# Optimization experiments

Measured on AMD Instinct MI355X. Metric: run time of the kernel, lower is better.

## Reference

```python
import jax, jax.numpy as jnp
import numpy as np

N_NODES = 100000


def gcn_conv(x, edge_index, W, b, n_nodes):
    """PyG GCNConv: add self-loops, symmetric deg norm, linear, scatter-add, bias."""
    self_loops = jnp.arange(n_nodes, dtype=edge_index.dtype)
    src = jnp.concatenate([edge_index[0], self_loops])  # [E+N]
    dst = jnp.concatenate([edge_index[1], self_loops])  # [E+N]
    xw = x @ W  # [N, out]
    deg = jax.ops.segment_sum(jnp.ones_like(dst, dtype=xw.dtype), dst, num_segments=n_nodes)
    deg_inv_sqrt = jnp.where(deg > 0, jax.lax.rsqrt(deg), 0.0)
    norm = deg_inv_sqrt[src] * deg_inv_sqrt[dst]  # [E+N]
    msg = xw[src] * norm[:, None]                 # [E+N, out]
    out = jax.ops.segment_sum(msg, dst, num_segments=n_nodes)
    return out + b


def setup_inputs() -> dict:
    key = jax.random.key(0)
    ks = jax.random.split(key, 8)
    n, e, d_in, h = N_NODES, 3200000, 128, 16
    x = jax.random.normal(ks[0], (n, d_in), dtype=jnp.float32)
    edge_index = jax.random.randint(ks[1], (2, e), 0, n, dtype=jnp.int64)
    W1 = jax.random.normal(ks[2], (d_in, h), dtype=jnp.float32) / np.sqrt(d_in)
    b1 = jnp.zeros((h,), dtype=jnp.float32)
    W2 = jax.random.normal(ks[3], (h, h), dtype=jnp.float32) / np.sqrt(h)
    b2 = jnp.zeros((h,), dtype=jnp.float32)
    W_lin = jax.random.normal(ks[4], (h, 1), dtype=jnp.float32) / np.sqrt(h)
    b_lin = jnp.zeros((1,), dtype=jnp.float32)
    return {"x": x, "edge_index": edge_index, "W1": W1, "b1": b1,
            "W2": W2, "b2": b2, "W_lin": W_lin, "b_lin": b_lin}


def reference(x, edge_index, W1, b1, W2, b2, W_lin, b_lin):
    n = x.shape[0]
    h = gcn_conv(x, edge_index, W1, b1, n)
    h = jax.nn.relu(h)
    # dropout is identity in eval mode (training=False)
    h = gcn_conv(h, edge_index, W2, b2, n)
    h = jax.nn.relu(h)
    out = h @ W_lin + b_lin  # [N, 1]
    return out.squeeze(-1)   # [N]
```

## Files before the change

kernel.cpp:

```cpp
#include <hip/hip_runtime.h>

#define DIN 128
#define HDIM 16
#define NB 256
#define BDIV_MAX 416
#define CAP 13312
#define BIN_EPT 16

__device__ __forceinline__ float4 f4add(float4 a, float4 b) {
    return make_float4(a.x + b.x, a.y + b.y, a.z + b.z, a.w + b.w);
}

__device__ __forceinline__ int load_idx(const void* ei, long long i, int is64) {
    return is64 ? (int)((const long long*)ei)[i] : ((const int*)ei)[i];
}

__global__ __launch_bounds__(256) void k_main(const void* __restrict__ ei, long long E,
                                              int bdiv, int* __restrict__ bcur,
                                              unsigned int* __restrict__ recs,
                                              const float* __restrict__ x,
                                              const float* __restrict__ W1,
                                              float* __restrict__ y1,
                                              int n, int nbin) {
    __shared__ int cnt[NB];
    __shared__ int base[NB];
    __shared__ float Ws[DIN * HDIM];
    int tid = threadIdx.x;
    if ((int)blockIdx.x < nbin) {
        unsigned probe = ((const unsigned*)ei)[1 + 2 * (tid & 63)];
        int is64 = (__ballot(probe != 0) == 0ull) ? 1 : 0;
        if (tid < NB) cnt[tid] = 0;
        __syncthreads();
        long long e0 = (long long)blockIdx.x * (256 * BIN_EPT);
        int s[BIN_EPT], d[BIN_EPT], b[BIN_EPT];
#pragma unroll
        for (int i = 0; i < BIN_EPT; i++) {
            long long e = e0 + (long long)i * 256 + tid;
            if (e < E) {
                s[i] = load_idx(ei, e, is64);
                d[i] = load_idx(ei, E + e, is64);
                b[i] = (int)((unsigned)d[i] / (unsigned)bdiv);
                atomicAdd(&cnt[b[i]], 1);
            } else {
                b[i] = -1;
            }
        }
        __syncthreads();
        if (tid < NB) {
            base[tid] = atomicAdd(&bcur[tid], cnt[tid]);
            cnt[tid] = 0;
        }
        __syncthreads();
#pragma unroll
        for (int i = 0; i < BIN_EPT; i++) {
            if (b[i] >= 0) {
                int off = atomicAdd(&cnt[b[i]], 1);
                int pos = base[b[i]] + off;
                if (pos < CAP) {
                    unsigned int dloc = (unsigned)(d[i] - b[i] * bdiv);
                    recs[(size_t)b[i] * CAP + pos] = (dloc << 18) | (unsigned)s[i];
                }
            }
        }
    } else {
        for (int i = tid; i < DIN * HDIM; i += 256) Ws[i] = W1[i];
        __syncthreads();
        int node = ((int)blockIdx.x - nbin) * 256 + tid;
        if (node >= n) return;
        float acc[HDIM];
#pragma unroll
        for (int f = 0; f < HDIM; f++) acc[f] = 0.f;
        const float4* xr = (const float4*)(x + (size_t)node * DIN);
#pragma unroll 8
        for (int k4 = 0; k4 < DIN / 4; k4++) {
            float4 xv = xr[k4];
            int k = k4 * 4;
#pragma unroll
            for (int f = 0; f < HDIM; f++) {
                acc[f] += xv.x * Ws[(k + 0) * HDIM + f];
                acc[f] += xv.y * Ws[(k + 1) * HDIM + f];
                acc[f] += xv.z * Ws[(k + 2) * HDIM + f];
                acc[f] += xv.w * Ws[(k + 3) * HDIM + f];
            }
        }
        float4* yr = (float4*)(y1 + (size_t)node * HDIM);
#pragma unroll
        for (int q = 0; q < 4; q++)
            yr[q] = make_float4(acc[q * 4 + 0], acc[q * 4 + 1],
                                acc[q * 4 + 2], acc[q * 4 + 3]);
    }
}

__global__ __launch_bounds__(512) void k_prep(const unsigned int* __restrict__ recs,
                                              const int* __restrict__ bcur,
                                              float* __restrict__ dis,
                                              unsigned int* __restrict__ meta,
                                              int* __restrict__ col,
                                              float* __restrict__ y1,
                                              int bdiv, int n) {
    __shared__ int cnt_sh[BDIV_MAX];
    __shared__ int sc[512];
    __shared__ unsigned short buf[CAP];
    int tid = threadIdx.x;
    int b = blockIdx.x;
    int lo = b * bdiv; if (lo > n) lo = n;
    int hi = lo + bdiv; if (hi > n) hi = n;
    int nd = hi - lo;
    if (tid < nd) cnt_sh[tid] = 0;
    __syncthreads();
    int m = bcur[b]; if (m > CAP) m = CAP;
    const unsigned int* r = recs + (size_t)b * CAP;
    for (int i = tid; i < m; i += 512)
        atomicAdd(&cnt_sh[r[i] >> 18], 1);
    __syncthreads();
    int v = (tid < nd) ? cnt_sh[tid] : 0;
    sc[tid] = v;
    __syncthreads();
    for (int off = 1; off < 512; off <<= 1) {
        int t = (tid >= off) ? sc[tid - off] : 0;
        __syncthreads();
        sc[tid] += t;
        __syncthreads();
    }
    float dv_t = 0.f;
    if (tid < nd) {
        int excl = sc[tid] - v;
        dv_t = rsqrtf((float)v + 1.0f);
        dis[lo + tid] = dv_t;
        meta[lo + tid] = ((unsigned)(b * CAP + excl) << 10) | (unsigned)v;
        cnt_sh[tid] = excl;
    }
    __syncthreads();
    for (int i = tid; i < m; i += 512) {
        int pos = atomicAdd(&cnt_sh[r[i] >> 18], 1);
        buf[pos] = (unsigned short)i;
    }
    __syncthreads();
    for (int i = tid; i < m; i += 512)
        col[b * CAP + i] = (int)(r[buf[i]] & 0x3FFFFu);
    int q = tid & 3;
    int slot = tid >> 2;
    float4* yv = (float4*)y1;
    for (int j = slot; j < nd; j += 128) {
        float dvj = __shfl(dv_t, 0, 1);
        (void)dvj;
        int node = lo + j;
        float dv = dis[node];
        float4 t = yv[(size_t)node * 4 + q];
        yv[(size_t)node * 4 + q] =
            make_float4(t.x * dv, t.y * dv, t.z * dv, t.w * dv);
    }
}

__global__ __launch_bounds__(256) void k_gather1(const unsigned int* __restrict__ meta,
                                                 const int* __restrict__ col,
                                                 const float* __restrict__ y1,
                                                 const float* __restrict__ dis,
                                                 const float* __restrict__ b1,
                                                 const float* __restrict__ W2,
                                                 float* __restrict__ y2, int n) {
    __shared__ float4 Ws4[HDIM][4];
    if (threadIdx.x < HDIM * 4)
        ((float4*)Ws4)[threadIdx.x] = ((const float4*)W2)[threadIdx.x];
    __syncthreads();
    int ln = threadIdx.x >> 2;
    int q  = threadIdx.x & 3;
    int node = blockIdx.x * 64 + ln;
    if (node >= n) return;
    unsigned mt = meta[node];
    int start = (int)(mt >> 10);
    int end   = start + (int)(mt & 1023u);
    const float4* yv = (const float4*)y1;
    float4 a0 = make_float4(0.f, 0.f, 0.f, 0.f), a1 = a0, a2 = a0, a3 = a0;
    int e = start;
    for (; e + 16 <= end; e += 16) {
        int c0 = col[e + q], c1 = col[e + 4 + q],
            c2 = col[e + 8 + q], c3 = col[e + 12 + q];
        int s[16];
#pragma unroll
        for (int k = 0; k < 4; k++) {
            s[k]      = __shfl(c0, k, 4);
            s[4 + k]  = __shfl(c1, k, 4);
            s[8 + k]  = __shfl(c2, k, 4);
            s[12 + k] = __shfl(c3, k, 4);
        }
        float4 v[16];
#pragma unroll
        for (int k = 0; k < 16; k++) v[k] = yv[(size_t)s[k] * 4 + q];
#pragma unroll
        for (int k = 0; k < 16; k += 4) {
            a0 = f4add(a0, v[k + 0]); a1 = f4add(a1, v[k + 1]);
            a2 = f4add(a2, v[k + 2]); a3 = f4add(a3, v[k + 3]);
        }
    }
    for (; e + 4 <= end; e += 4) {
        int c0 = col[e + q];
        int s0 = __shfl(c0, 0, 4), s1 = __shfl(c0, 1, 4),
            s2 = __shfl(c0, 2, 4), s3 = __shfl(c0, 3, 4);
        float4 v0 = yv[(size_t)s0 * 4 + q];
        float4 v1 = yv[(size_t)s1 * 4 + q];
        float4 v2 = yv[(size_t)s2 * 4 + q];
        float4 v3 = yv[(size_t)s3 * 4 + q];
        a0 = f4add(a0, v0); a1 = f4add(a1, v1);
        a2 = f4add(a2, v2); a3 = f4add(a3, v3);
    }
    for (; e < end; e++)
        a0 = f4add(a0, yv[(size_t)col[e] * 4 + q]);
    float4 acc = f4add(f4add(a0, a1), f4add(a2, a3));
    acc = f4add(acc, yv[(size_t)node * 4 + q]);
    float dv = dis[node];
    float4 bb = ((const float4*)b1)[q];
    float4 h;
    h.x = fmaxf(dv * acc.x + bb.x, 0.f);
    h.y = fmaxf(dv * acc.y + bb.y, 0.f);
    h.z = fmaxf(dv * acc.z + bb.z, 0.f);
    h.w = fmaxf(dv * acc.w + bb.w, 0.f);
    float4 o = make_float4(0.f, 0.f, 0.f, 0.f);
#pragma unroll
    for (int k = 0; k < 4; k++) {
        float4 hk;
        hk.x = __shfl(h.x, k, 4); hk.y = __shfl(h.y, k, 4);
        hk.z = __shfl(h.z, k, 4); hk.w = __shfl(h.w, k, 4);
        float hv[4] = {hk.x, hk.y, hk.z, hk.w};
#pragma unroll
        for (int c = 0; c < 4; c++) {
            float4 w = Ws4[k * 4 + c][q];
            o.x += hv[c] * w.x; o.y += hv[c] * w.y;
            o.z += hv[c] * w.z; o.w += hv[c] * w.w;
        }
    }
    ((float4*)y2)[(size_t)node * 4 + q] =
        make_float4(o.x * dv, o.y * dv, o.z * dv, o.w * dv);
}

__global__ __launch_bounds__(256) void k_gather2(const unsigned int* __restrict__ meta,
                                                 const int* __restrict__ col,
                                                 const float* __restrict__ y2,
                                                 const float* __restrict__ dis,
                                                 const float* __restrict__ b2,
                                                 const float* __restrict__ Wlin,
                                                 const float* __restrict__ blin,
                                                 float* __restrict__ out, int n) {
    int ln = threadIdx.x >> 2;
    int q  = threadIdx.x & 3;
    int node = blockIdx.x * 64 + ln;
    if (node >= n) return;
    unsigned mt = meta[node];
    int start = (int)(mt >> 10);
    int end   = start + (int)(mt & 1023u);
    const float4* yv = (const float4*)y2;
    float4 a0 = make_float4(0.f, 0.f, 0.f, 0.f), a1 = a0, a2 = a0, a3 = a0;
    int e = start;
    for (; e + 16 <= end; e += 16) {
        int c0 = col[e + q], c1 = col[e + 4 + q],
            c2 = col[e + 8 + q], c3 = col[e + 12 + q];
        int s[16];
#pragma unroll
        for (int k = 0; k < 4; k++) {
            s[k]      = __shfl(c0, k, 4);
            s[4 + k]  = __shfl(c1, k, 4);
            s[8 + k]  = __shfl(c2, k, 4);
            s[12 + k] = __shfl(c3, k, 4);
        }
        float4 v[16];
#pragma unroll
        for (int k = 0; k < 16; k++) v[k] = yv[(size_t)s[k] * 4 + q];
#pragma unroll
        for (int k = 0; k < 16; k += 4) {
            a0 = f4add(a0, v[k + 0]); a1 = f4add(a1, v[k + 1]);
            a2 = f4add(a2, v[k + 2]); a3 = f4add(a3, v[k + 3]);
        }
    }
    for (; e + 4 <= end; e += 4) {
        int c0 = col[e + q];
        int s0 = __shfl(c0, 0, 4), s1 = __shfl(c0, 1, 4),
            s2 = __shfl(c0, 2, 4), s3 = __shfl(c0, 3, 4);
        float4 v0 = yv[(size_t)s0 * 4 + q];
        float4 v1 = yv[(size_t)s1 * 4 + q];
        float4 v2 = yv[(size_t)s2 * 4 + q];
        float4 v3 = yv[(size_t)s3 * 4 + q];
        a0 = f4add(a0, v0); a1 = f4add(a1, v1);
        a2 = f4add(a2, v2); a3 = f4add(a3, v3);
    }
    for (; e < end; e++)
        a0 = f4add(a0, yv[(size_t)col[e] * 4 + q]);
    float4 acc = f4add(f4add(a0, a1), f4add(a2, a3));
    acc = f4add(acc, yv[(size_t)node * 4 + q]);
    float dv = dis[node];
    float4 bb = ((const float4*)b2)[q];
    float4 wl = ((const float4*)Wlin)[q];
    float v = 0.f;
    v += fmaxf(dv * acc.x + bb.x, 0.f) * wl.x;
    v += fmaxf(dv * acc.y + bb.y, 0.f) * wl.y;
    v += fmaxf(dv * acc.z + bb.z, 0.f) * wl.z;
    v += fmaxf(dv * acc.w + bb.w, 0.f) * wl.w;
    v += __shfl_xor(v, 1, 4);
    v += __shfl_xor(v, 2, 4);
    if (q == 0) out[node] = v + blin[0];
}

extern "C" void kernel_launch(void* const* d_in, const int* in_sizes, int n_in,
                              void* d_out, int out_size, void* d_ws, size_t ws_size,
                              hipStream_t stream) {
    const float* x    = (const float*)d_in[0];
    const void*  ei   = d_in[1];
    const float* W1   = (const float*)d_in[2];
    const float* b1   = (const float*)d_in[3];
    const float* W2   = (const float*)d_in[4];
    const float* b2   = (const float*)d_in[5];
    const float* Wlin = (const float*)d_in[6];
    const float* blin = (const float*)d_in[7];
    float* out = (float*)d_out;

    const int n = in_sizes[0] / DIN;
    const long long E = in_sizes[1] / 2;
    const int bdiv = (n + NB - 1) / NB;

    char* ws = (char*)d_ws;
    size_t off = 0;
    auto alloc = [&](size_t bytes) { char* p = ws + off; off += (bytes + 255) & ~(size_t)255; return p; };
    int*   bcur   = (int*)alloc(NB * 4);
    float* dis    = (float*)alloc((size_t)n * 4);
    unsigned int* meta = (unsigned int*)alloc((size_t)n * 4);
    float* y1     = (float*)alloc((size_t)n * HDIM * 4);
    size_t region_elems = (size_t)NB * CAP;
    if (region_elems < (size_t)n * HDIM) region_elems = (size_t)n * HDIM;
    char*  region = alloc(region_elems * 4);
    unsigned int* recs = (unsigned int*)region;
    float* y2     = (float*)region;
    int*   col    = (int*)alloc((size_t)NB * CAP * 4);

    const int nb_xw  = (n + 255) / 256;
    const int nb_bin = (int)((E + 256 * BIN_EPT - 1) / (256 * BIN_EPT));
    const int nb_g   = (n + 63) / 64;

    hipMemsetAsync(bcur, 0, NB * sizeof(int), stream);
    k_main<<<nb_bin + nb_xw, 256, 0, stream>>>(ei, E, bdiv, bcur, recs, x, W1, y1, n, nb_bin);
    k_prep<<<NB, 512, 0, stream>>>(recs, bcur, dis, meta, col, y1, bdiv, n);
    k_gather1<<<nb_g, 256, 0, stream>>>(meta, col, y1, dis, b1, W2, y2, n);
    k_gather2<<<nb_g, 256, 0, stream>>>(meta, col, y2, dis, b2, Wlin, blin, out, n);
}
```

Baseline: 229.8 us.

## Fuse all GCN stages into one persistent cooperative kernel with grid syncs

Replaces the memset plus four separate kernel launches with a single cooperative persistent kernel that runs binning/XW, bucket prep, and both gathers as phases separated by grid-wide syncs. Bucket count grows from 256 to 512 with a smaller per-bucket capacity, blocks go to 512 threads, and the gather unroll drops from 16 to 8. The aim is to remove launch gaps and tail effects between stages. The cost is grid-sync overhead and a grid capped at 1024 blocks, which may limit parallelism in the gather phases. The old multi-kernel path is kept as a fallback if the cooperative launch fails.

```diff
diff --git a/kernel.cpp b/kernel.cpp
--- a/kernel.cpp
+++ b/kernel.cpp
@@ -1,11 +1,13 @@
 #include <hip/hip_runtime.h>
+#include <hip/hip_cooperative_groups.h>
+
+namespace cg = cooperative_groups;
 
 #define DIN 128
 #define HDIM 16
-#define NB 256
-#define BDIV_MAX 416
-#define CAP 13312
-#define BIN_EPT 16
+#define NB2 512
+#define CAP2 7168
+#define SMEM_BYTES 18432
 
 __device__ __forceinline__ float4 f4add(float4 a, float4 b) {
     return make_float4(a.x + b.x, a.y + b.y, a.z + b.z, a.w + b.w);
@@ -15,101 +17,86 @@
     return is64 ? (int)((const long long*)ei)[i] : ((const int*)ei)[i];
 }
 
-__global__ __launch_bounds__(256) void k_main(const void* __restrict__ ei, long long E,
-                                              int bdiv, int* __restrict__ bcur,
-                                              unsigned int* __restrict__ recs,
-                                              const float* __restrict__ x,
-                                              const float* __restrict__ W1,
-                                              float* __restrict__ y1,
-                                              int n, int nbin) {
-    __shared__ int cnt[NB];
-    __shared__ int base[NB];
-    __shared__ float Ws[DIN * HDIM];
-    int tid = threadIdx.x;
-    if ((int)blockIdx.x < nbin) {
-        unsigned probe = ((const unsigned*)ei)[1 + 2 * (tid & 63)];
-        int is64 = (__ballot(probe != 0) == 0ull) ? 1 : 0;
-        if (tid < NB) cnt[tid] = 0;
-        __syncthreads();
-        long long e0 = (long long)blockIdx.x * (256 * BIN_EPT);
-        int s[BIN_EPT], d[BIN_EPT], b[BIN_EPT];
-#pragma unroll
-        for (int i = 0; i < BIN_EPT; i++) {
-            long long e = e0 + (long long)i * 256 + tid;
-            if (e < E) {
-                s[i] = load_idx(ei, e, is64);
-                d[i] = load_idx(ei, E + e, is64);
-                b[i] = (int)((unsigned)d[i] / (unsigned)bdiv);
-                atomicAdd(&cnt[b[i]], 1);
-            } else {
-                b[i] = -1;
+__device__ __forceinline__ void bin_unit(int u, int tid, char* smem,
+        const void* ei, long long E, int bdiv, int* bcur, unsigned* recs) {
+    int* cnt  = (int*)smem;
+    int* base = cnt + 512;
+    unsigned probe = ((const unsigned*)ei)[1 + 2 * (tid & 63)];
+    int is64 = (__ballot(probe != 0) == 0ull) ? 1 : 0;
+    cnt[tid] = 0;
+    __syncthreads();
+    long long e0 = (long long)u * 4096;
+    int s[8], d[8], bb[8];
+#pragma unroll
+    for (int i = 0; i < 8; i++) {
+        long long e = e0 + i * 512 + tid;
+        if (e < E) {
+            s[i] = load_idx(ei, e, is64);
+            d[i] = load_idx(ei, E + e, is64);
+            bb[i] = (int)((unsigned)d[i] / (unsigned)bdiv);
+            atomicAdd(&cnt[bb[i]], 1);
+        } else bb[i] = -1;
+    }
+    __syncthreads();
+    base[tid] = atomicAdd(&bcur[tid], cnt[tid]);
+    cnt[tid] = 0;
+    __syncthreads();
+#pragma unroll
+    for (int i = 0; i < 8; i++) {
+        if (bb[i] >= 0) {
+            int off = atomicAdd(&cnt[bb[i]], 1);
+            int pos = base[bb[i]] + off;
+            if (pos < CAP2) {
+                unsigned dloc = (unsigned)(d[i] - bb[i] * bdiv);
+                recs[(size_t)bb[i] * CAP2 + pos] = (dloc << 18) | (unsigned)s[i];
             }
         }
-        __syncthreads();
-        if (tid < NB) {
-            base[tid] = atomicAdd(&bcur[tid], cnt[tid]);
-            cnt[tid] = 0;
-        }
-        __syncthreads();
-#pragma unroll
-        for (int i = 0; i < BIN_EPT; i++) {
-            if (b[i] >= 0) {
-                int off = atomicAdd(&cnt[b[i]], 1);
-                int pos = base[b[i]] + off;
-                if (pos < CAP) {
-                    unsigned int dloc = (unsigned)(d[i] - b[i] * bdiv);
-                    recs[(size_t)b[i] * CAP + pos] = (dloc << 18) | (unsigned)s[i];
-                }
-            }
-        }
-    } else {
-        for (int i = tid; i < DIN * HDIM; i += 256) Ws[i] = W1[i];
-        __syncthreads();
-        int node = ((int)blockIdx.x - nbin) * 256 + tid;
-        if (node >= n) return;
-        float acc[HDIM];
-#pragma unroll
-        for (int f = 0; f < HDIM; f++) acc[f] = 0.f;
-        const float4* xr = (const float4*)(x + (size_t)node * DIN);
+    }
+}
+
+__device__ __forceinline__ void xw_unit(int urel, int tid, char* smem,
+        const float* x, const float* W1, float* y1, int n) {
+    float* Ws = (float*)smem;
+    for (int i = tid; i < DIN * HDIM; i += 512) Ws[i] = W1[i];
+    __syncthreads();
+    int node = urel * 512 + tid;
+    if (node >= n) return;
+    float acc[HDIM];
+#pragma unroll
+    for (int f = 0; f < HDIM; f++) acc[f] = 0.f;
+    const float4* xr = (const float4*)(x + (size_t)node * DIN);
 #pragma unroll 8
-        for (int k4 = 0; k4 < DIN / 4; k4++) {
-            float4 xv = xr[k4];
-            int k = k4 * 4;
-#pragma unroll
-            for (int f = 0; f < HDIM; f++) {
-                acc[f] += xv.x * Ws[(k + 0) * HDIM + f];
-                acc[f] += xv.y * Ws[(k + 1) * HDIM + f];
-                acc[f] += xv.z * Ws[(k + 2) * HDIM + f];
-                acc[f] += xv.w * Ws[(k + 3) * HDIM + f];
-            }
-        }
-        float4* yr = (float4*)(y1 + (size_t)node * HDIM);
-#pragma unroll
-        for (int q = 0; q < 4; q++)
-            yr[q] = make_float4(acc[q * 4 + 0], acc[q * 4 + 1],
-                                acc[q * 4 + 2], acc[q * 4 + 3]);
-    }
-}
-
-__global__ __launch_bounds__(512) void k_prep(const unsigned int* __restrict__ recs,
-                                              const int* __restrict__ bcur,
-                                              float* __restrict__ dis,
-                                              unsigned int* __restrict__ meta,
-                                              int* __restrict__ col,
-                                              float* __restrict__ y1,
-                                              int bdiv, int n) {
-    __shared__ int cnt_sh[BDIV_MAX];
-    __shared__ int sc[512];
-    __shared__ unsigned short buf[CAP];
-    int tid = threadIdx.x;
-    int b = blockIdx.x;
+    for (int k4 = 0; k4 < DIN / 4; k4++) {
+        float4 xv = xr[k4];
+        int k = k4 * 4;
+#pragma unroll
+        for (int f = 0; f < HDIM; f++) {
+            acc[f] += xv.x * Ws[(k + 0) * HDIM + f];
+            acc[f] += xv.y * Ws[(k + 1) * HDIM + f];
+            acc[f] += xv.z * Ws[(k + 2) * HDIM + f];
+            acc[f] += xv.w * Ws[(k + 3) * HDIM + f];
+        }
+    }
+    float4* yr = (float4*)(y1 + (size_t)node * HDIM);
+#pragma unroll
+    for (int q = 0; q < 4; q++)
+        yr[q] = make_float4(acc[q * 4 + 0], acc[q * 4 + 1],
+                            acc[q * 4 + 2], acc[q * 4 + 3]);
+}
+
+__device__ __forceinline__ void prep_bucket(int b, int tid, char* smem,
+        const unsigned* recs, const int* bcur, float* dis, unsigned* meta,
+        int* col, float* y1, int bdiv, int n) {
+    int* cnt_sh = (int*)smem;
+    int* sc     = cnt_sh + 512;
+    unsigned short* buf = (unsigned short*)(sc + 512);
     int lo = b * bdiv; if (lo > n) lo = n;
     int hi = lo + bdiv; if (hi > n) hi = n;
     int nd = hi - lo;
     if (tid < nd) cnt_sh[tid] = 0;
     __syncthreads();
-    int m = bcur[b]; if (m > CAP) m = CAP;
-    const unsigned int* r = recs + (size_t)b * CAP;
+    int m = bcur[b]; if (m > CAP2) m = CAP2;
+    const unsigned* r = recs + (size_t)b * CAP2;
     for (int i = tid; i < m; i += 512)
         atomicAdd(&cnt_sh[r[i] >> 18], 1);
     __syncthreads();
@@ -122,12 +109,10 @@
         sc[tid] += t;
         __syncthreads();
     }
-    float dv_t = 0.f;
     if (tid < nd) {
         int excl = sc[tid] - v;
-        dv_t = rsqrtf((float)v + 1.0f);
-        dis[lo + tid] = dv_t;
-        meta[lo + tid] = ((unsigned)(b * CAP + excl) << 10) | (unsigned)v;
+        dis[lo + tid] = rsqrtf((float)v + 1.0f);
+        meta[lo + tid] = ((unsigned)(b * CAP2 + excl) << 10) | (unsigned)v;
         cnt_sh[tid] = excl;
     }
     __syncthreads();
@@ -137,13 +122,10 @@
     }
     __syncthreads();
     for (int i = tid; i < m; i += 512)
-        col[b * CAP + i] = (int)(r[buf[i]] & 0x3FFFFu);
-    int q = tid & 3;
-    int slot = tid >> 2;
+        col[b * CAP2 + i] = (int)(r[buf[i]] & 0x3FFFFu);
+    int q = tid & 3, slot = tid >> 2;
     float4* yv = (float4*)y1;
     for (int j = slot; j < nd; j += 128) {
-        float dvj = __shfl(dv_t, 0, 1);
-        (void)dvj;
         int node = lo + j;
         float dv = dis[node];
         float4 t = yv[(size_t)node * 4 + q];
@@ -152,20 +134,11 @@
     }
 }
 
-__global__ __launch_bounds__(256) void k_gather1(const unsigned int* __restrict__ meta,
-                                                 const int* __restrict__ col,
-                                                 const float* __restrict__ y1,
-                                                 const float* __restrict__ dis,
-                                                 const float* __restrict__ b1,
-                                                 const float* __restrict__ W2,
-                                                 float* __restrict__ y2, int n) {
-    __shared__ float4 Ws4[HDIM][4];
-    if (threadIdx.x < HDIM * 4)
-        ((float4*)Ws4)[threadIdx.x] = ((const float4*)W2)[threadIdx.x];
-    __syncthreads();
-    int ln = threadIdx.x >> 2;
-    int q  = threadIdx.x & 3;
-    int node = blockIdx.x * 64 + ln;
+__device__ __forceinline__ void gather1_unit(int u, int tid, const float4* ws4,
+        const unsigned* meta, const int* col, const float* y1,
+        const float* dis, const float* b1, float* y2, int n) {
+    int ln = tid >> 2, q = tid & 3;
+    int node = u * 128 + ln;
     if (node >= n) return;
     unsigned mt = meta[node];
     int start = (int)(mt >> 10);
@@ -173,25 +146,21 @@
     const float4* yv = (const float4*)y1;
     float4 a0 = make_float4(0.f, 0.f, 0.f, 0.f), a1 = a0, a2 = a0, a3 = a0;
     int e = start;
-    for (; e + 16 <= end; e += 16) {
-        int c0 = col[e + q], c1 = col[e + 4 + q],
-            c2 = col[e + 8 + q], c3 = col[e + 12 + q];
-        int s[16];
+    for (; e + 8 <= end; e += 8) {
+        int c0 = col[e + q], c1 = col[e + 4 + q];
+        int s[8];
 #pragma unroll
         for (int k = 0; k < 4; k++) {
-            s[k]      = __shfl(c0, k, 4);
-            s[4 + k]  = __shfl(c1, k, 4);
-            s[8 + k]  = __shfl(c2, k, 4);
-            s[12 + k] = __shfl(c3, k, 4);
-        }
-        float4 v[16];
-#pragma unroll
-        for (int k = 0; k < 16; k++) v[k] = yv[(size_t)s[k] * 4 + q];
-#pragma unroll
-        for (int k = 0; k < 16; k += 4) {
-            a0 = f4add(a0, v[k + 0]); a1 = f4add(a1, v[k + 1]);
-            a2 = f4add(a2, v[k + 2]); a3 = f4add(a3, v[k + 3]);
-        }
+            s[k]     = __shfl(c0, k, 4);
+            s[4 + k] = __shfl(c1, k, 4);
+        }
+        float4 v[8];
+#pragma unroll
+        for (int k = 0; k < 8; k++) v[k] = yv[(size_t)s[k] * 4 + q];
+        a0 = f4add(a0, v[0]); a1 = f4add(a1, v[1]);
+        a2 = f4add(a2, v[2]); a3 = f4add(a3, v[3]);
+        a0 = f4add(a0, v[4]); a1 = f4add(a1, v[5]);
+        a2 = f4add(a2, v[6]); a3 = f4add(a3, v[7]);
     }
     for (; e + 4 <= end; e += 4) {
         int c0 = col[e + q];
@@ -224,7 +193,7 @@
         float hv[4] = {hk.x, hk.y, hk.z, hk.w};
 #pragma unroll
         for (int c = 0; c < 4; c++) {
-            float4 w = Ws4[k * 4 + c][q];
+            float4 w = ws4[(k * 4 + c) * 4 + q];
             o.x += hv[c] * w.x; o.y += hv[c] * w.y;
             o.z += hv[c] * w.z; o.w += hv[c] * w.w;
         }
@@ -233,17 +202,12 @@
         make_float4(o.x * dv, o.y * dv, o.z * dv, o.w * dv);
 }
 
-__global__ __launch_bounds__(256) void k_gather2(const unsigned int* __restrict__ meta,
-                                                 const int* __restrict__ col,
-                                                 const float* __restrict__ y2,
-                                                 const float* __restrict__ dis,
-                                                 const float* __restrict__ b2,
-                                                 const float* __restrict__ Wlin,
-                                                 const float* __restrict__ blin,
-                                                 float* __restrict__ out, int n) {
-    int ln = threadIdx.x >> 2;
-    int q  = threadIdx.x & 3;
-    int node = blockIdx.x * 64 + ln;
+__device__ __forceinline__ void gather2_unit(int u, int tid,
+        const unsigned* meta, const int* col, const float* y2,
+        const float* dis, const float* b2, const float* Wlin,
+        const float* blin, float* out, int n) {
+    int ln = tid >> 2, q = tid & 3;
+    int node = u * 128 + ln;
     if (node >= n) return;
     unsigned mt = meta[node];
     int start = (int)(mt >> 10);
@@ -251,25 +215,21 @@
     const float4* yv = (const float4*)y2;
     float4 a0 = make_float4(0.f, 0.f, 0.f, 0.f), a1 = a0, a2 = a0, a3 = a0;
     int e = start;
-    for (; e + 16 <= end; e += 16) {
-        int c0 = col[e + q], c1 = col[e + 4 + q],
-            c2 = col[e + 8 + q], c3 = col[e + 12 + q];
-        int s[16];
+    for (; e + 8 <= end; e += 8) {
+        int c0 = col[e + q], c1 = col[e + 4 + q];
+        int s[8];
 #pragma unroll
         for (int k = 0; k < 4; k++) {
-            s[k]      = __shfl(c0, k, 4);
-            s[4 + k]  = __shfl(c1, k, 4);
-            s[8 + k]  = __shfl(c2, k, 4);
-            s[12 + k] = __shfl(c3, k, 4);
-        }
-        float4 v[16];
-#pragma unroll
-        for (int k = 0; k < 16; k++) v[k] = yv[(size_t)s[k] * 4 + q];
-#pragma unroll
-        for (int k = 0; k < 16; k += 4) {
-            a0 = f4add(a0, v[k + 0]); a1 = f4add(a1, v[k + 1]);
-            a2 = f4add(a2, v[k + 2]); a3 = f4add(a3, v[k + 3]);
-        }
+            s[k]     = __shfl(c0, k, 4);
+            s[4 + k] = __shfl(c1, k, 4);
+        }
+        float4 v[8];
+#pragma unroll
+        for (int k = 0; k < 8; k++) v[k] = yv[(size_t)s[k] * 4 + q];
+        a0 = f4add(a0, v[0]); a1 = f4add(a1, v[1]);
+        a2 = f4add(a2, v[2]); a3 = f4add(a3, v[3]);
+        a0 = f4add(a0, v[4]); a1 = f4add(a1, v[5]);
+        a2 = f4add(a2, v[6]); a3 = f4add(a3, v[7]);
     }
     for (; e + 4 <= end; e += 4) {
         int c0 = col[e + q];
@@ -299,44 +259,135 @@
     if (q == 0) out[node] = v + blin[0];
 }
 
+__global__ __launch_bounds__(512, 4) void k_mega(
+        const void* ei, long long E, int bdiv, int* bcur,
+        unsigned* recs ,
+        const float* x, const float* W1, float* y1,
+        float* dis, unsigned* meta, int* col,
+        const float* b1, const float* W2,
+        const float* b2, const float* Wlin, const float* blin,
+        float* out, int n, int nbin, int nxw) {
+    __shared__ __align__(16) char smem[SMEM_BYTES];
+    cg::grid_group g = cg::this_grid();
+    int tid = threadIdx.x, bid = blockIdx.x, gsz = gridDim.x;
+    for (int i = bid * 512 + tid; i < NB2; i += gsz * 512) bcur[i] = 0;
+    g.sync();
+    int total = nbin + nxw;
+    for (int u = bid; u < total; u += gsz) {
+        if (u < nbin) bin_unit(u, tid, smem, ei, E, bdiv, bcur, recs);
+        else          xw_unit(u - nbin, tid, smem, x, W1, y1, n);
+        __syncthreads();
+    }
+    g.sync();
+    for (int b = bid; b < NB2; b += gsz) {
+        prep_bucket(b, tid, smem, recs, bcur, dis, meta, col, y1, bdiv, n);
+        __syncthreads();
+    }
+    g.sync();
+    float4* ws4 = (float4*)smem;
+    if (tid < 64) ws4[tid] = ((const float4*)W2)[tid];
+    __syncthreads();
+    float* y2 = (float*)recs;
+    int units = (n + 127) >> 7;
+    for (int u = bid; u < units; u += gsz)
+        gather1_unit(u, tid, ws4, meta, col, y1, dis, b1, y2, n);
+    g.sync();
+    for (int u = bid; u < units; u += gsz)
+        gather2_unit(u, tid, meta, col, y2, dis, b2, Wlin, blin, out, n);
+}
+
+__global__ __launch_bounds__(512) void f_main(const void* ei, long long E,
+        int bdiv, int* bcur, unsigned* recs, const float* x,
+        const float* W1, float* y1, int n, int nbin) {
+    __shared__ __align__(16) char smem[SMEM_BYTES];
+    int u = blockIdx.x;
+    if (u < nbin) bin_unit(u, threadIdx.x, smem, ei, E, bdiv, bcur, recs);
+    else          xw_unit(u - nbin, threadIdx.x, smem, x, W1, y1, n);
+}
+
+__global__ __launch_bounds__(512) void f_prep(const unsigned* recs,
+        const int* bcur, float* dis, unsigned* meta, int* col,
+        float* y1, int bdiv, int n) {
+    __shared__ __align__(16) char smem[SMEM_BYTES];
+    prep_bucket(blockIdx.x, threadIdx.x, smem, recs, bcur, dis, meta, col,
+                y1, bdiv, n);
+}
+
+__global__ __launch_bounds__(512) void f_g1(const unsigned* meta,
+        const int* col, const float* y1, const float* dis,
+        const float* b1, const float* W2, float* y2, int n) {
+    __shared__ __align__(16) float4 ws4[64];
+    if (threadIdx.x < 64) ws4[threadIdx.x] = ((const float4*)W2)[threadIdx.x];
+    __syncthreads();
+    gather1_unit(blockIdx.x, threadIdx.x, ws4, meta, col, y1, dis, b1, y2, n);
+}
+
+__global__ __launch_bounds__(512) void f_g2(const unsigned* meta,
+        const int* col, const float* y2, const float* dis,
+        const float* b2, const float* Wlin, const float* blin,
+        float* out, int n) {
+    gather2_unit(blockIdx.x, threadIdx.x, meta, col, y2, dis, b2, Wlin,
+                 blin, out, n);
+}
+
 extern "C" void kernel_launch(void* const* d_in, const int* in_sizes, int n_in,
                               void* d_out, int out_size, void* d_ws, size_t ws_size,
                               hipStream_t stream) {
     const float* x    = (const float*)d_in[0];
     const void*  ei   = d_in[1];
+    const float* b1   = (const float*)d_in[3];
     const float* W1   = (const float*)d_in[2];
-    const float* b1   = (const float*)d_in[3];
     const float* W2   = (const float*)d_in[4];
     const float* b2   = (const float*)d_in[5];
     const float* Wlin = (const float*)d_in[6];
     const float* blin = (const float*)d_in[7];
     float* out = (float*)d_out;
 
-    const int n = in_sizes[0] / DIN;
-    const long long E = in_sizes[1] / 2;
-    const int bdiv = (n + NB - 1) / NB;
+    int n = in_sizes[0] / DIN;
+    long long E = in_sizes[1] / 2;
+    int bdiv = (n + NB2 - 1) / NB2;
 
     char* ws = (char*)d_ws;
     size_t off = 0;
     auto alloc = [&](size_t bytes) { char* p = ws + off; off += (bytes + 255) & ~(size_t)255; return p; };
-    int*   bcur   = (int*)alloc(NB * 4);
-    float* dis    = (float*)alloc((size_t)n * 4);
-    unsigned int* meta = (unsigned int*)alloc((size_t)n * 4);
-    float* y1     = (float*)alloc((size_t)n * HDIM * 4);
-    size_t region_elems = (size_t)NB * CAP;
+    int*      bcur = (int*)alloc(NB2 * 4);
+    float*    dis  = (float*)alloc((size_t)n * 4);
+    unsigned* meta = (unsigned*)alloc((size_t)n * 4);
+    float*    y1   = (float*)alloc((size_t)n * HDIM * 4);
+    size_t region_elems = (size_t)NB2 * CAP2;
     if (region_elems < (size_t)n * HDIM) region_elems = (size_t)n * HDIM;
-    char*  region = alloc(region_elems * 4);
-    unsigned int* recs = (unsigned int*)region;
-    float* y2     = (float*)region;
-    int*   col    = (int*)alloc((size_t)NB * CAP * 4);
-
-    const int nb_xw  = (n + 255) / 256;
-    const int nb_bin = (int)((E + 256 * BIN_EPT - 1) / (256 * BIN_EPT));
-    const int nb_g   = (n + 63) / 64;
-
-    hipMemsetAsync(bcur, 0, NB * sizeof(int), stream);
-    k_main<<<nb_bin + nb_xw, 256, 0, stream>>>(ei, E, bdiv, bcur, recs, x, W1, y1, n, nb_bin);
-    k_prep<<<NB, 512, 0, stream>>>(recs, bcur, dis, meta, col, y1, bdiv, n);
-    k_gather1<<<nb_g, 256, 0, stream>>>(meta, col, y1, dis, b1, W2, y2, n);
-    k_gather2<<<nb_g, 256, 0, stream>>>(meta, col, y2, dis, b2, Wlin, blin, out, n);
-}
+    char* region = alloc(region_elems * 4);
+    unsigned* recs = (unsigned*)region;
+    int*      col  = (int*)alloc((size_t)NB2 * CAP2 * 4);
+
+    int nbin  = (int)((E + 4095) / 4096);
+    int nxw   = (n + 511) / 512;
+    int units = (n + 127) / 128;
+
+    void* args[] = { (void*)&ei, (void*)&E, (void*)&bdiv, (void*)&bcur,
+                     (void*)&recs, (void*)&x, (void*)&W1, (void*)&y1,
+                     (void*)&dis, (void*)&meta, (void*)&col,
+                     (void*)&b1, (void*)&W2, (void*)&b2, (void*)&Wlin,
+                     (void*)&blin, (void*)&out, (void*)&n, (void*)&nbin,
+                     (void*)&nxw };
+
+    int nbpc = 0;
+    hipError_t occ = hipOccupancyMaxActiveBlocksPerMultiprocessor(
+        &nbpc, (const void*)k_mega, 512, 0);
+    int grid = (occ == hipSuccess && nbpc > 0) ? nbpc * 256 : 256;
+    if (grid > 1024) grid = 1024;
+
+    hipError_t st = hipLaunchCooperativeKernel((void*)k_mega, dim3(grid),
+                                               dim3(512), args, 0, stream);
+    if (st != hipSuccess) {
+        hipMemsetAsync(bcur, 0, NB2 * sizeof(int), stream);
+        f_main<<<nbin + nxw, 512, 0, stream>>>(ei, E, bdiv, bcur, recs,
+                                               x, W1, y1, n, nbin);
+        f_prep<<<NB2, 512, 0, stream>>>(recs, bcur, dis, meta, col, y1,
+                                        bdiv, n);
+        f_g1<<<units, 512, 0, stream>>>(meta, col, y1, dis, b1, W2,
+                                        (float*)recs, n);
+        f_g2<<<units, 512, 0, stream>>>(meta, col, (float*)recs, dis, b2,
+                                        Wlin, blin, out, n);
+    }
+}
```

Result: slower. 386.2 us (+68.1%).

## Pad CSR rows to multiples of four with a zero dummy node

Applied to the files above, without the earlier changes.

Each node's adjacency row in the CSR built in k_prep is padded to a multiple of four entries. Padding slots point to an extra all-zero row at index n, which is added to y1 and y2. The gather kernels can then load column indices as aligned int4 vectors and drop the scalar tail loop. The cost is extra sentinel-fill work in prep, a slightly larger col buffer, and wasted gathers of the zero row.

```diff
diff --git a/kernel.cpp b/kernel.cpp
--- a/kernel.cpp
+++ b/kernel.cpp
@@ -3,8 +3,8 @@
 #define DIN 128
 #define HDIM 16
 #define NB 256
-#define BDIV_MAX 416
 #define CAP 13312
+#define CAPC 14848
 #define BIN_EPT 16
 
 __device__ __forceinline__ float4 f4add(float4 a, float4 b) {
@@ -66,7 +66,14 @@
         for (int i = tid; i < DIN * HDIM; i += 256) Ws[i] = W1[i];
         __syncthreads();
         int node = ((int)blockIdx.x - nbin) * 256 + tid;
-        if (node >= n) return;
+        if (node > n) return;
+        float4* yr = (float4*)(y1 + (size_t)node * HDIM);
+        if (node == n) {
+            float4 z = make_float4(0.f, 0.f, 0.f, 0.f);
+#pragma unroll
+            for (int q = 0; q < 4; q++) yr[q] = z;
+            return;
+        }
         float acc[HDIM];
 #pragma unroll
         for (int f = 0; f < HDIM; f++) acc[f] = 0.f;
@@ -83,7 +90,6 @@
                 acc[f] += xv.w * Ws[(k + 3) * HDIM + f];
             }
         }
-        float4* yr = (float4*)(y1 + (size_t)node * HDIM);
 #pragma unroll
         for (int q = 0; q < 4; q++)
             yr[q] = make_float4(acc[q * 4 + 0], acc[q * 4 + 1],
@@ -98,23 +104,24 @@
                                               int* __restrict__ col,
                                               float* __restrict__ y1,
                                               int bdiv, int n) {
-    __shared__ int cnt_sh[BDIV_MAX];
+    __shared__ int cnt_sh[512];
     __shared__ int sc[512];
-    __shared__ unsigned short buf[CAP];
+    __shared__ unsigned short buf[CAPC];
     int tid = threadIdx.x;
     int b = blockIdx.x;
     int lo = b * bdiv; if (lo > n) lo = n;
     int hi = lo + bdiv; if (hi > n) hi = n;
     int nd = hi - lo;
-    if (tid < nd) cnt_sh[tid] = 0;
+    cnt_sh[tid] = 0;
     __syncthreads();
     int m = bcur[b]; if (m > CAP) m = CAP;
     const unsigned int* r = recs + (size_t)b * CAP;
     for (int i = tid; i < m; i += 512)
         atomicAdd(&cnt_sh[r[i] >> 18], 1);
     __syncthreads();
-    int v = (tid < nd) ? cnt_sh[tid] : 0;
-    sc[tid] = v;
+    int v  = (tid < nd) ? cnt_sh[tid] : 0;
+    int pv = (v + 3) & ~3;
+    sc[tid] = pv;
     __syncthreads();
     for (int off = 1; off < 512; off <<= 1) {
         int t = (tid >= off) ? sc[tid - off] : 0;
@@ -122,28 +129,27 @@
         sc[tid] += t;
         __syncthreads();
     }
-    float dv_t = 0.f;
+    int ptot = sc[511];
     if (tid < nd) {
-        int excl = sc[tid] - v;
-        dv_t = rsqrtf((float)v + 1.0f);
-        dis[lo + tid] = dv_t;
-        meta[lo + tid] = ((unsigned)(b * CAP + excl) << 10) | (unsigned)v;
+        int excl = sc[tid] - pv;
+        dis[lo + tid] = rsqrtf((float)v + 1.0f);
+        meta[lo + tid] = ((unsigned)(b * CAPC + excl) << 10) | (unsigned)v;
         cnt_sh[tid] = excl;
     }
+    for (int i = tid; i < ptot; i += 512) buf[i] = 0xFFFFu;
     __syncthreads();
     for (int i = tid; i < m; i += 512) {
         int pos = atomicAdd(&cnt_sh[r[i] >> 18], 1);
         buf[pos] = (unsigned short)i;
     }
     __syncthreads();
-    for (int i = tid; i < m; i += 512)
-        col[b * CAP + i] = (int)(r[buf[i]] & 0x3FFFFu);
-    int q = tid & 3;
-    int slot = tid >> 2;
+    for (int i = tid; i < ptot; i += 512) {
+        unsigned short bi = buf[i];
+        col[b * CAPC + i] = (bi == 0xFFFFu) ? n : (int)(r[bi] & 0x3FFFFu);
+    }
+    int q = tid & 3, slot = tid >> 2;
     float4* yv = (float4*)y1;
     for (int j = slot; j < nd; j += 128) {
-        float dvj = __shfl(dv_t, 0, 1);
-        (void)dvj;
         int node = lo + j;
         float dv = dis[node];
         float4 t = yv[(size_t)node * 4 + q];
@@ -163,26 +169,27 @@
     if (threadIdx.x < HDIM * 4)
         ((float4*)Ws4)[threadIdx.x] = ((const float4*)W2)[threadIdx.x];
     __syncthreads();
+    if (blockIdx.x == 0 && threadIdx.x < 4)
+        ((float4*)y2)[(size_t)n * 4 + threadIdx.x] = make_float4(0.f, 0.f, 0.f, 0.f);
     int ln = threadIdx.x >> 2;
     int q  = threadIdx.x & 3;
     int node = blockIdx.x * 64 + ln;
     if (node >= n) return;
     unsigned mt = meta[node];
     int start = (int)(mt >> 10);
-    int end   = start + (int)(mt & 1023u);
+    int endp  = start + (((int)(mt & 1023u) + 3) & ~3);
     const float4* yv = (const float4*)y1;
     float4 a0 = make_float4(0.f, 0.f, 0.f, 0.f), a1 = a0, a2 = a0, a3 = a0;
     int e = start;
-    for (; e + 16 <= end; e += 16) {
-        int c0 = col[e + q], c1 = col[e + 4 + q],
-            c2 = col[e + 8 + q], c3 = col[e + 12 + q];
+    for (; e + 16 <= endp; e += 16) {
+        int4 c4 = *(const int4*)(col + e + 4 * q);
         int s[16];
 #pragma unroll
-        for (int k = 0; k < 4; k++) {
-            s[k]      = __shfl(c0, k, 4);
-            s[4 + k]  = __shfl(c1, k, 4);
-            s[8 + k]  = __shfl(c2, k, 4);
-            s[12 + k] = __shfl(c3, k, 4);
+        for (int j = 0; j < 4; j++) {
+            s[4 * j + 0] = __shfl(c4.x, j, 4);
+            s[4 * j + 1] = __shfl(c4.y, j, 4);
+            s[4 * j + 2] = __shfl(c4.z, j, 4);
+            s[4 * j + 3] = __shfl(c4.w, j, 4);
         }
         float4 v[16];
 #pragma unroll
@@ -193,19 +200,15 @@
             a2 = f4add(a2, v[k + 2]); a3 = f4add(a3, v[k + 3]);
         }
     }
-    for (; e + 4 <= end; e += 4) {
-        int c0 = col[e + q];
-        int s0 = __shfl(c0, 0, 4), s1 = __shfl(c0, 1, 4),
-            s2 = __shfl(c0, 2, 4), s3 = __shfl(c0, 3, 4);
-        float4 v0 = yv[(size_t)s0 * 4 + q];
-        float4 v1 = yv[(size_t)s1 * 4 + q];
-        float4 v2 = yv[(size_t)s2 * 4 + q];
-        float4 v3 = yv[(size_t)s3 * 4 + q];
+    for (; e < endp; e += 4) {
+        int4 c4 = *(const int4*)(col + e);
+        float4 v0 = yv[(size_t)c4.x * 4 + q];
+        float4 v1 = yv[(size_t)c4.y * 4 + q];
+        float4 v2 = yv[(size_t)c4.z * 4 + q];
+        float4 v3 = yv[(size_t)c4.w * 4 + q];
         a0 = f4add(a0, v0); a1 = f4add(a1, v1);
         a2 = f4add(a2, v2); a3 = f4add(a3, v3);
     }
-    for (; e < end; e++)
-        a0 = f4add(a0, yv[(size_t)col[e] * 4 + q]);
     float4 acc = f4add(f4add(a0, a1), f4add(a2, a3));
     acc = f4add(acc, yv[(size_t)node * 4 + q]);
     float dv = dis[node];
@@ -247,20 +250,19 @@
     if (node >= n) return;
     unsigned mt = meta[node];
     int start = (int)(mt >> 10);
-    int end   = start + (int)(mt & 1023u);
+    int endp  = start + (((int)(mt & 1023u) + 3) & ~3);
     const float4* yv = (const float4*)y2;
     float4 a0 = make_float4(0.f, 0.f, 0.f, 0.f), a1 = a0, a2 = a0, a3 = a0;
     int e = start;
-    for (; e + 16 <= end; e += 16) {
-        int c0 = col[e + q], c1 = col[e + 4 + q],
-            c2 = col[e + 8 + q], c3 = col[e + 12 + q];
+    for (; e + 16 <= endp; e += 16) {
+        int4 c4 = *(const int4*)(col + e + 4 * q);
         int s[16];
 #pragma unroll
-        for (int k = 0; k < 4; k++) {
-            s[k]      = __shfl(c0, k, 4);
-            s[4 + k]  = __shfl(c1, k, 4);
-            s[8 + k]  = __shfl(c2, k, 4);
-            s[12 + k] = __shfl(c3, k, 4);
+        for (int j = 0; j < 4; j++) {
+            s[4 * j + 0] = __shfl(c4.x, j, 4);
+            s[4 * j + 1] = __shfl(c4.y, j, 4);
+            s[4 * j + 2] = __shfl(c4.z, j, 4);
+            s[4 * j + 3] = __shfl(c4.w, j, 4);
         }
         float4 v[16];
 #pragma unroll
@@ -271,19 +273,15 @@
             a2 = f4add(a2, v[k + 2]); a3 = f4add(a3, v[k + 3]);
         }
     }
-    for (; e + 4 <= end; e += 4) {
-        int c0 = col[e + q];
-        int s0 = __shfl(c0, 0, 4), s1 = __shfl(c0, 1, 4),
-            s2 = __shfl(c0, 2, 4), s3 = __shfl(c0, 3, 4);
-        float4 v0 = yv[(size_t)s0 * 4 + q];
-        float4 v1 = yv[(size_t)s1 * 4 + q];
-        float4 v2 = yv[(size_t)s2 * 4 + q];
-        float4 v3 = yv[(size_t)s3 * 4 + q];
+    for (; e < endp; e += 4) {
+        int4 c4 = *(const int4*)(col + e);
+        float4 v0 = yv[(size_t)c4.x * 4 + q];
+        float4 v1 = yv[(size_t)c4.y * 4 + q];
+        float4 v2 = yv[(size_t)c4.z * 4 + q];
+        float4 v3 = yv[(size_t)c4.w * 4 + q];
         a0 = f4add(a0, v0); a1 = f4add(a1, v1);
         a2 = f4add(a2, v2); a3 = f4add(a3, v3);
     }
-    for (; e < end; e++)
-        a0 = f4add(a0, yv[(size_t)col[e] * 4 + q]);
     float4 acc = f4add(f4add(a0, a1), f4add(a2, a3));
     acc = f4add(acc, yv[(size_t)node * 4 + q]);
     float dv = dis[node];
@@ -322,15 +320,15 @@
     int*   bcur   = (int*)alloc(NB * 4);
     float* dis    = (float*)alloc((size_t)n * 4);
     unsigned int* meta = (unsigned int*)alloc((size_t)n * 4);
-    float* y1     = (float*)alloc((size_t)n * HDIM * 4);
+    float* y1     = (float*)alloc((size_t)(n + 1) * HDIM * 4);
     size_t region_elems = (size_t)NB * CAP;
-    if (region_elems < (size_t)n * HDIM) region_elems = (size_t)n * HDIM;
+    if (region_elems < (size_t)(n + 1) * HDIM) region_elems = (size_t)(n + 1) * HDIM;
     char*  region = alloc(region_elems * 4);
     unsigned int* recs = (unsigned int*)region;
     float* y2     = (float*)region;
-    int*   col    = (int*)alloc((size_t)NB * CAP * 4);
-
-    const int nb_xw  = (n + 255) / 256;
+    int*   col    = (int*)alloc((size_t)NB * CAPC * 4);
+
+    const int nb_xw  = (n + 1 + 255) / 256;
     const int nb_bin = (int)((E + 256 * BIN_EPT - 1) / (256 * BIN_EPT));
     const int nb_g   = (n + 63) / 64;
 
```

Measured after the change: 228.1 us. Within noise of the previous version (-0.7%).
